# Optimization experiments

Measured on AMD Instinct MI355X. Metric: run time of the kernel, lower is better.

The kernel has to match this reference:

```python
import jax, jax.numpy as jnp
import numpy as np

B, N, DIM, H = 32, 3136, 768, 12
C = DIM // H  # head_dim = 64


def setup_inputs() -> dict:
    key = jax.random.key(0)
    k1, k2, k3, k4 = jax.random.split(key, 4)
    x = jax.random.normal(k1, (B, N, DIM), dtype=jnp.float32)
    # Linear weights stored as (in, out); qkv has no bias (qkv_bias=False)
    w_qkv = jax.random.normal(k2, (DIM, 3 * DIM), dtype=jnp.float32) * (1.0 / np.sqrt(DIM))
    w_proj = jax.random.normal(k3, (DIM, DIM), dtype=jnp.float32) * (1.0 / np.sqrt(DIM))
    b_proj = jax.random.normal(k4, (DIM,), dtype=jnp.float32) * 0.01
    return {"x": x, "w_qkv": w_qkv, "w_proj": w_proj, "b_proj": b_proj}


def reference(x, w_qkv, w_proj, b_proj):
    # qkv projection: [B,N,3*DIM] -> [3,B,H,N,C]
    qkv = (x @ w_qkv).reshape(B, N, 3, H, C).transpose(2, 0, 3, 1, 4)
    q, k, v = qkv[0], qkv[1], qkv[2]
    # Efficient (linear) attention: softmax q over channel dim, k over token dim
    q = jax.nn.softmax(q, axis=-1)                      # [B,H,N,C], softmax over C
    kt = jax.nn.softmax(k.transpose(0, 1, 3, 2), axis=-1)  # [B,H,C,N], softmax over N
    context = jnp.einsum('bhcn,bhnd->bhcd', kt, v)      # [B,H,C,C]
    out = jnp.einsum('bhnc,bhcd->bhnd', q, context)     # [B,H,N,C]
    out = out.transpose(0, 2, 1, 3).reshape(B, N, DIM)  # [B,N,DIM]
    return out @ w_proj + b_proj
```

## Files before the change

kernel.cpp:

```cpp
#include <hip/hip_runtime.h>
#include <hip/hip_bf16.h>

typedef __attribute__((ext_vector_type(8))) short bf16x8;
typedef __attribute__((ext_vector_type(4))) float f32x4;

constexpr int BATCH = 32, SEQ = 3136, DIM = 768, NH = 12, HD = 64;
constexpr int M_TOT = BATCH * SEQ;
constexpr int QKVC  = 3 * DIM;
constexpr int GK    = 768;

__device__ __forceinline__ float bf2f(unsigned short u) {
  union { unsigned int i; float f; } x; x.i = ((unsigned int)u) << 16; return x.f;
}
__device__ __forceinline__ unsigned short f2bf(float f) {
  union { float f; unsigned int i; } x; x.f = f;
  unsigned int r = x.i + 0x7FFFu + ((x.i >> 16) & 1u);
  return (unsigned short)(r >> 16);
}
__device__ __forceinline__ unsigned int pack2(float lo, float hi) {
  return (unsigned int)f2bf(lo) | ((unsigned int)f2bf(hi) << 16);
}
__device__ __forceinline__ void gload_lds16(const unsigned short* g, unsigned short* l) {
  __builtin_amdgcn_global_load_lds(
      (const __attribute__((address_space(1))) void*)g,
      (__attribute__((address_space(3))) void*)l, 16, 0, 0);
}

#define BARX()  asm volatile("s_barrier" ::: "memory")
#define LGKM0() asm volatile("s_waitcnt lgkmcnt(0)" ::: "memory")
#define VM4()   asm volatile("s_waitcnt vmcnt(4)" ::: "memory")
#define SB0()   __builtin_amdgcn_sched_barrier(0)

__global__ void conv_kernel(const float* __restrict__ in, unsigned short* __restrict__ out, long n) {
  long i = ((long)blockIdx.x * blockDim.x + threadIdx.x) * 8;
  long stride = (long)gridDim.x * blockDim.x * 8;
  for (; i < n; i += stride) {
    float4 a = *(const float4*)(in + i);
    float4 b = *(const float4*)(in + i + 4);
    uint4 o;
    o.x = pack2(a.x, a.y); o.y = pack2(a.z, a.w);
    o.z = pack2(b.x, b.y); o.w = pack2(b.z, b.w);
    *(uint4*)(out + i) = o;
  }
}

__global__ void transp_kernel(const float* __restrict__ w, unsigned short* __restrict__ wt, int K, int N) {
  __shared__ float tile[32][33];
  int n0 = blockIdx.x * 32, k0 = blockIdx.y * 32;
  int tx = threadIdx.x, ty = threadIdx.y;
  #pragma unroll
  for (int i = 0; i < 32; i += 8)
    tile[ty + i][tx] = w[(size_t)(k0 + ty + i) * N + n0 + tx];
  __syncthreads();
  #pragma unroll
  for (int i = 0; i < 32; i += 8)
    wt[(size_t)(n0 + ty + i) * K + k0 + tx] = f2bf(tile[tx][ty + i]);
}

__device__ __forceinline__ void stage_half(const unsigned short* __restrict__ G, long row0, int col0,
                                           unsigned short* ldsHalf, int t) {
  int r = t >> 2;
  int gslot = (t & 3) ^ ((t >> 3) & 3);
  char* dst = (char*)ldsHalf + ((t >> 6) << 10);
  gload_lds16(G + (row0 + r) * (long)GK + col0 + gslot * 8, (unsigned short*)dst);
  gload_lds16(G + (row0 + 128 + r) * (long)GK + col0 + gslot * 8, (unsigned short*)(dst + 8192));
}
__device__ __forceinline__ bf16x8 frag(const unsigned short* half, int r, int ko) {
  return *(const bf16x8*)((const char*)half + r * 64 + ((((ko >> 3) ^ ((r >> 1) & 3))) << 4));
}

#define MM16G(Q,A0,A1,A2,A3,B0,B1,B2,B3) do { \
  acc[(Q)+0][0]=__builtin_amdgcn_mfma_f32_16x16x32_bf16(B0,A0,acc[(Q)+0][0],0,0,0); \
  acc[(Q)+0][1]=__builtin_amdgcn_mfma_f32_16x16x32_bf16(B1,A0,acc[(Q)+0][1],0,0,0); \
  acc[(Q)+0][2]=__builtin_amdgcn_mfma_f32_16x16x32_bf16(B2,A0,acc[(Q)+0][2],0,0,0); \
  acc[(Q)+0][3]=__builtin_amdgcn_mfma_f32_16x16x32_bf16(B3,A0,acc[(Q)+0][3],0,0,0); \
  acc[(Q)+1][0]=__builtin_amdgcn_mfma_f32_16x16x32_bf16(B0,A1,acc[(Q)+1][0],0,0,0); \
  acc[(Q)+1][1]=__builtin_amdgcn_mfma_f32_16x16x32_bf16(B1,A1,acc[(Q)+1][1],0,0,0); \
  acc[(Q)+1][2]=__builtin_amdgcn_mfma_f32_16x16x32_bf16(B2,A1,acc[(Q)+1][2],0,0,0); \
  acc[(Q)+1][3]=__builtin_amdgcn_mfma_f32_16x16x32_bf16(B3,A1,acc[(Q)+1][3],0,0,0); \
  acc[(Q)+2][0]=__builtin_amdgcn_mfma_f32_16x16x32_bf16(B0,A2,acc[(Q)+2][0],0,0,0); \
  acc[(Q)+2][1]=__builtin_amdgcn_mfma_f32_16x16x32_bf16(B1,A2,acc[(Q)+2][1],0,0,0); \
  acc[(Q)+2][2]=__builtin_amdgcn_mfma_f32_16x16x32_bf16(B2,A2,acc[(Q)+2][2],0,0,0); \
  acc[(Q)+2][3]=__builtin_amdgcn_mfma_f32_16x16x32_bf16(B3,A2,acc[(Q)+2][3],0,0,0); \
  acc[(Q)+3][0]=__builtin_amdgcn_mfma_f32_16x16x32_bf16(B0,A3,acc[(Q)+3][0],0,0,0); \
  acc[(Q)+3][1]=__builtin_amdgcn_mfma_f32_16x16x32_bf16(B1,A3,acc[(Q)+3][1],0,0,0); \
  acc[(Q)+3][2]=__builtin_amdgcn_mfma_f32_16x16x32_bf16(B2,A3,acc[(Q)+3][2],0,0,0); \
  acc[(Q)+3][3]=__builtin_amdgcn_mfma_f32_16x16x32_bf16(B3,A3,acc[(Q)+3][3],0,0,0); \
} while (0)

#define KTILE_X(BUF, MA2, NB2, C2, MA3, NB3, C3) { \
  const unsigned short* Ah0 = &lds[BUF][0][0][0]; \
  const unsigned short* Ah1 = &lds[BUF][0][1][0]; \
  const unsigned short* Bh1 = &lds[BUF][1][1][0]; \
  const unsigned short* Ah0n = &lds[(BUF) ^ 1][0][0][0]; \
  const unsigned short* Bh0n = &lds[(BUF) ^ 1][1][0][0]; \
   \
  LGKM0(); SB0(); \
  __builtin_amdgcn_s_setprio(1); MM16G(0, a0, a1, a2, a3, b0, b1, b2, b3); \
  __builtin_amdgcn_s_setprio(0); SB0(); \
  a4 = frag(Ah0, ra + 64, ko); a5 = frag(Ah0, ra + 80, ko); \
  a6 = frag(Ah0, ra + 96, ko); a7 = frag(Ah0, ra + 112, ko); \
  b4 = frag(Bh1, rb, ko); b5 = frag(Bh1, rb + 16, ko); \
  stage_half(A, MA2, C2, &lds[(BUF) ^ 1][0][1][0], t); \
  BARX(); \
   \
  LGKM0(); SB0(); \
  __builtin_amdgcn_s_setprio(1); MM16G(4, a4, a5, a6, a7, b0, b1, b2, b3); \
  __builtin_amdgcn_s_setprio(0); SB0(); \
  a0 = frag(Ah1, ra,      ko); a1 = frag(Ah1, ra + 16, ko); \
  a2 = frag(Ah1, ra + 32, ko); a3 = frag(Ah1, ra + 48, ko); \
  b6 = frag(Bh1, rb + 32, ko); b7 = frag(Bh1, rb + 48, ko); \
  stage_half(Bt, NB2, C2, &lds[(BUF) ^ 1][1][1][0], t); \
  VM4(); BARX(); \
   \
  LGKM0(); SB0(); \
  __builtin_amdgcn_s_setprio(1); MM16G(0, a0, a1, a2, a3, b4, b5, b6, b7); \
  __builtin_amdgcn_s_setprio(0); SB0(); \
  a4 = frag(Ah1, ra + 64, ko); a5 = frag(Ah1, ra + 80, ko); \
  a6 = frag(Ah1, ra + 96, ko); a7 = frag(Ah1, ra + 112, ko); \
  b0 = frag(Bh0n, rb, ko); b1 = frag(Bh0n, rb + 16, ko); \
  stage_half(A, MA3, C3, &lds[BUF][0][0][0], t); \
  BARX(); \
   \
  LGKM0(); SB0(); \
  __builtin_amdgcn_s_setprio(1); MM16G(4, a4, a5, a6, a7, b4, b5, b6, b7); \
  __builtin_amdgcn_s_setprio(0); SB0(); \
  a0 = frag(Ah0n, ra,      ko); a1 = frag(Ah0n, ra + 16, ko); \
  a2 = frag(Ah0n, ra + 32, ko); a3 = frag(Ah0n, ra + 48, ko); \
  b2 = frag(Bh0n, rb + 32, ko); b3 = frag(Bh0n, rb + 48, ko); \
  stage_half(Bt, NB3, C3, &lds[BUF][1][0][0], t); \
  VM4(); BARX(); \
}

template<int OUTMODE, int NT>
__global__ __launch_bounds__(512, 2) void gemm256p(const unsigned short* __restrict__ A,
                                                   const unsigned short* __restrict__ Bt,
                                                   void* __restrict__ Cp,
                                                   const float* __restrict__ bias,
                                                   int Nld, int TPX) {
  __shared__ unsigned short lds[2][2][2][8192];
  int t = threadIdx.x, lane = t & 63, wid = t >> 6;
  int wm = wid >> 2, wn = wid & 3;
  int bid = (int)blockIdx.x;
  int xcd = bid & 7, slot = bid >> 3;
  int tau = xcd * TPX + slot;
  int tend = (xcd + 1) * TPX;
  int fl = lane & 15, ko = (lane >> 4) * 8;
  int ra = wm * 128 + fl, rb = wn * 64 + fl;
  f32x4 acc[8][4];
  bf16x8 a0, a1, a2, a3, a4, a5, a6, a7, b0, b1, b2, b3, b4, b5, b6, b7;
  {
    long m0 = (long)(tau / NT) * 256, n0 = (long)(tau % NT) * 256;
    stage_half(A,  m0, 0,  &lds[0][0][0][0], t);
    stage_half(Bt, n0, 0,  &lds[0][1][0][0], t);
    stage_half(A,  m0, 32, &lds[0][0][1][0], t);
    stage_half(Bt, n0, 32, &lds[0][1][1][0], t);
    stage_half(A,  m0, 64, &lds[1][0][0][0], t);
    stage_half(Bt, n0, 64, &lds[1][1][0][0], t);
    VM4(); BARX();
    a0 = frag(&lds[0][0][0][0], ra,      ko); a1 = frag(&lds[0][0][0][0], ra + 16, ko);
    a2 = frag(&lds[0][0][0][0], ra + 32, ko); a3 = frag(&lds[0][0][0][0], ra + 48, ko);
    b0 = frag(&lds[0][1][0][0], rb,      ko); b1 = frag(&lds[0][1][0][0], rb + 16, ko);
    b2 = frag(&lds[0][1][0][0], rb + 32, ko); b3 = frag(&lds[0][1][0][0], rb + 48, ko);
  }
  #pragma unroll 1
  for (; tau < tend; tau += 32) {
    long m0 = (long)(tau / NT) * 256, n0 = (long)(tau % NT) * 256;
    int tn = (tau + 32 < tend) ? tau + 32 : tau;
    long m0n = (long)(tn / NT) * 256, n0n = (long)(tn % NT) * 256;
    #pragma unroll
    for (int i = 0; i < 8; ++i)
      #pragma unroll
      for (int j2 = 0; j2 < 4; ++j2) acc[i][j2] = (f32x4){0.f, 0.f, 0.f, 0.f};
    #pragma unroll 1
    for (int j = 0; j < 10; j += 2) {
      KTILE_X(0, m0, n0, j * 64 + 96,  m0, n0, j * 64 + 128);
      KTILE_X(1, m0, n0, j * 64 + 160, m0, n0, j * 64 + 192);
    }
    KTILE_X(0, m0,  n0,  736, m0n, n0n, 0);
    KTILE_X(1, m0n, n0n, 32,  m0n, n0n, 64);
    int q4 = (lane >> 4) * 4;
    #pragma unroll
    for (int mf = 0; mf < 8; ++mf) {
      long row = m0 + wm * 128 + mf * 16 + fl;
      #pragma unroll
      for (int nf = 0; nf < 4; ++nf) {
        int col = (int)n0 + wn * 64 + nf * 16 + q4;
        if (OUTMODE == 0) {
          unsigned short* C = (unsigned short*)Cp;
          bool doexp = (n0 < 2 * DIM);
          float v0 = acc[mf][nf][0], v1 = acc[mf][nf][1], v2 = acc[mf][nf][2], v3 = acc[mf][nf][3];
          if (doexp) { v0 = __expf(v0); v1 = __expf(v1); v2 = __expf(v2); v3 = __expf(v3); }
          uint2 o; o.x = pack2(v0, v1); o.y = pack2(v2, v3);
          *(uint2*)(C + (size_t)row * Nld + col) = o;
        } else {
          float* C = (float*)Cp;
          float4 bb = *(const float4*)(bias + col);
          float4 o = { acc[mf][nf][0] + bb.x, acc[mf][nf][1] + bb.y,
                       acc[mf][nf][2] + bb.z, acc[mf][nf][3] + bb.w };
          *(float4*)(C + (size_t)row * Nld + col) = o;
        }
      }
    }
  }
}

__global__ void ctx_part(const unsigned short* __restrict__ qkv, float* __restrict__ part,
                         float* __restrict__ dpart) {
  int blk = blockIdx.x;
  int bh = blk / 7, ch = blk - bh * 7;
  int b = bh / NH, h = bh % NH;
  __shared__ unsigned short Et[64 * 40];
  __shared__ unsigned short Vt[64 * 40];
  __shared__ float denom[64];
  int t = threadIdx.x, lane = t & 63, w = t >> 6;
  if (t < 64) denom[t] = 0.0f;
  int nl = t >> 3, e0 = (t & 7) * 8;
  int ko = (lane >> 4) * 8, fl = lane & 15;
  size_t base = (size_t)b * SEQ * QKVC + (size_t)h * HD;
  float dp[8] = {};
  f32x4 acc[4] = {};
  int c0b = ch * 448;
  for (int c0 = c0b; c0 < c0b + 448; c0 += 32) {
    __syncthreads();
    size_t rb = base + (size_t)(c0 + nl) * QKVC;
    uint4 kvec = *(const uint4*)(qkv + rb + DIM + e0);
    uint4 vvec = *(const uint4*)(qkv + rb + 2 * DIM + e0);
    const unsigned short* kp = (const unsigned short*)&kvec;
    const unsigned short* vp = (const unsigned short*)&vvec;
    #pragma unroll
    for (int j = 0; j < 8; ++j) {
      dp[j] += bf2f(kp[j]);
      Et[(e0 + j) * 40 + nl] = kp[j];
      Vt[(e0 + j) * 40 + nl] = vp[j];
    }
    __syncthreads();
    bf16x8 af = *(const bf16x8*)(Et + (w * 16 + fl) * 40 + ko);
    #pragma unroll
    for (int nf = 0; nf < 4; ++nf) {
      bf16x8 bv = *(const bf16x8*)(Vt + (nf * 16 + fl) * 40 + ko);
      acc[nf] = __builtin_amdgcn_mfma_f32_16x16x32_bf16(af, bv, acc[nf], 0, 0, 0);
    }
  }
  #pragma unroll
  for (int j = 0; j < 8; ++j) atomicAdd(&denom[e0 + j], dp[j]);
  __syncthreads();
  int r0 = (lane >> 4) * 4;
  float* pp = part + (size_t)blk * 4096;
  #pragma unroll
  for (int nf = 0; nf < 4; ++nf)
    #pragma unroll
    for (int r = 0; r < 4; ++r) {
      int c = w * 16 + r0 + r;
      int d = nf * 16 + fl;
      pp[d * 64 + c] = acc[nf][r];
    }
  if (t < 64) dpart[blk * 64 + t] = denom[t];
}

__global__ void ctx_reduce(const float* __restrict__ part, const float* __restrict__ dpart,
                           unsigned short* __restrict__ ctxT) {
  int bh = blockIdx.x, t = threadIdx.x;
  const float* pp = part + (size_t)bh * 7 * 4096;
  const float* dd = dpart + (size_t)bh * 7 * 64;
  #pragma unroll
  for (int i = 0; i < 16; ++i) {
    int idx = i * 256 + t;
    float s = 0.f, ds = 0.f;
    #pragma unroll
    for (int c = 0; c < 7; ++c) {
      s += pp[c * 4096 + idx];
      ds += dd[c * 64 + (idx & 63)];
    }
    ctxT[(size_t)bh * 4096 + idx] = f2bf(s / ds);
  }
}

__global__ void pv_kernel(const unsigned short* __restrict__ qkv, const unsigned short* __restrict__ ctxT,
                          unsigned short* __restrict__ aout) {
  int bid = blockIdx.x;
  int bh = bid / 49, chunk = bid - bh * 49;
  int b = bh / NH, h = bh % NH;
  int n0 = chunk * 64;
  __shared__ unsigned short P[64 * 80];
  __shared__ unsigned short CT[64 * 80];
  __shared__ float srow[64];
  int t = threadIdx.x, lane = t & 63, w = t >> 6;
  int ko = (lane >> 4) * 8, fl = lane & 15;
  if (t < 64) srow[t] = 0.0f;
  {
    int d = t >> 2, cq = (t & 3) * 16;
    const uint4* src = (const uint4*)(ctxT + (size_t)bh * 4096 + d * 64 + cq);
    *(uint4*)(CT + d * 80 + cq) = src[0];
    *(uint4*)(CT + d * 80 + cq + 8) = src[1];
  }
  __syncthreads();
  {
    int nl = t >> 2, cq = (t & 3) * 16;
    size_t rb = (size_t)(b * SEQ + n0 + nl) * QKVC + h * HD + cq;
    uint4 q0 = *(const uint4*)(qkv + rb);
    uint4 q1 = *(const uint4*)(qkv + rb + 8);
    *(uint4*)(P + nl * 80 + cq) = q0;
    *(uint4*)(P + nl * 80 + cq + 8) = q1;
    const unsigned short* qp0 = (const unsigned short*)&q0;
    const unsigned short* qp1 = (const unsigned short*)&q1;
    float s = 0.0f;
    #pragma unroll
    for (int j = 0; j < 8; ++j) s += bf2f(qp0[j]) + bf2f(qp1[j]);
    atomicAdd(&srow[nl], s);
  }
  __syncthreads();
  f32x4 acc[4] = {};
  #pragma unroll
  for (int kk = 0; kk < 2; ++kk) {
    bf16x8 af = *(const bf16x8*)(P + (w * 16 + fl) * 80 + kk * 32 + ko);
    #pragma unroll
    for (int nf = 0; nf < 4; ++nf) {
      bf16x8 bv = *(const bf16x8*)(CT + (nf * 16 + fl) * 80 + kk * 32 + ko);
      acc[nf] = __builtin_amdgcn_mfma_f32_16x16x32_bf16(af, bv, acc[nf], 0, 0, 0);
    }
  }
  int r0 = (lane >> 4) * 4;
  #pragma unroll
  for (int nf = 0; nf < 4; ++nf)
    #pragma unroll
    for (int r = 0; r < 4; ++r) {
      int nlr = w * 16 + r0 + r;
      int d = nf * 16 + fl;
      float v = acc[nf][r] / srow[nlr];
      aout[(size_t)(b * SEQ + n0 + nlr) * DIM + h * HD + d] = f2bf(v);
    }
}

extern "C" void kernel_launch(void* const* d_in, const int* in_sizes, int n_in,
                              void* d_out, int out_size, void* d_ws, size_t ws_size,
                              hipStream_t stream) {
  const float* x      = (const float*)d_in[0];
  const float* w_qkv  = (const float*)d_in[1];
  const float* w_proj = (const float*)d_in[2];
  const float* b_proj = (const float*)d_in[3];
  char* ws = (char*)d_ws;
  unsigned short* x_bf    = (unsigned short*)(ws);
  unsigned short* wt_qkv  = (unsigned short*)(ws + 154140672);
  unsigned short* wt_proj = (unsigned short*)(ws + 157679616);
  unsigned short* qkv     = (unsigned short*)(ws + 158859264);
  unsigned short* ctxT    = (unsigned short*)(ws + 154140672);
  float* part  = (float*)(ws);
  float* dpart = (float*)(ws + 44040192);
  unsigned short* aout = (unsigned short*)(ws);

  conv_kernel<<<2048, 256, 0, stream>>>(x, x_bf, (long)M_TOT * DIM);
  transp_kernel<<<dim3(QKVC / 32, DIM / 32), dim3(32, 8), 0, stream>>>(w_qkv, wt_qkv, DIM, QKVC);
  transp_kernel<<<dim3(DIM / 32, DIM / 32), dim3(32, 8), 0, stream>>>(w_proj, wt_proj, DIM, DIM);
  gemm256p<0, 9><<<256, 512, 0, stream>>>(x_bf, wt_qkv, qkv, nullptr, QKVC, 441);
  ctx_part<<<BATCH * NH * 7, 256, 0, stream>>>(qkv, part, dpart);
  ctx_reduce<<<BATCH * NH, 256, 0, stream>>>(part, dpart, ctxT);
  pv_kernel<<<BATCH * NH * (SEQ / 64), 256, 0, stream>>>(qkv, ctxT, aout);
  gemm256p<1, 3><<<256, 512, 0, stream>>>(aout, wt_proj, (float*)d_out, b_proj, DIM, 147);
}
```

Baseline: 860.6 us.

## Interleave LDS fragment reads with MFMAs in GEMM and merge prep kernels

The GEMM k-tile body is restructured so global-to-LDS staging is issued at the start of each quarter step, and LDS fragment loads are interleaved between groups of four MFMAs. The vmcnt waits are loosened (vmcnt 6/8) to keep more loads in flight. The goal is to hide LDS read latency behind matrix work and deepen memory pipelining. Separately, the bf16 conversion and the two weight-transpose kernels are merged into one launch to cut launch overhead. The new wait counts and barrier placement change the synchronisation assumptions, which could introduce races if the in-flight counts are wrong.

```diff
diff --git a/kernel.cpp b/kernel.cpp
--- a/kernel.cpp
+++ b/kernel.cpp
@@ -28,33 +28,44 @@
 
 #define BARX()  asm volatile("s_barrier" ::: "memory")
 #define LGKM0() asm volatile("s_waitcnt lgkmcnt(0)" ::: "memory")
-#define VM4()   asm volatile("s_waitcnt vmcnt(4)" ::: "memory")
+#define VM8()   asm volatile("s_waitcnt vmcnt(8)" ::: "memory")
+#define VM6()   asm volatile("s_waitcnt vmcnt(6)" ::: "memory")
 #define SB0()   __builtin_amdgcn_sched_barrier(0)
 
-__global__ void conv_kernel(const float* __restrict__ in, unsigned short* __restrict__ out, long n) {
-  long i = ((long)blockIdx.x * blockDim.x + threadIdx.x) * 8;
-  long stride = (long)gridDim.x * blockDim.x * 8;
-  for (; i < n; i += stride) {
-    float4 a = *(const float4*)(in + i);
-    float4 b = *(const float4*)(in + i + 4);
-    uint4 o;
-    o.x = pack2(a.x, a.y); o.y = pack2(a.z, a.w);
-    o.z = pack2(b.x, b.y); o.w = pack2(b.z, b.w);
-    *(uint4*)(out + i) = o;
-  }
-}
-
-__global__ void transp_kernel(const float* __restrict__ w, unsigned short* __restrict__ wt, int K, int N) {
+__global__ void prep_kernel(const float* __restrict__ x, unsigned short* __restrict__ x_bf,
+                            const float* __restrict__ w_qkv, unsigned short* __restrict__ wt_qkv,
+                            const float* __restrict__ w_proj, unsigned short* __restrict__ wt_proj) {
   __shared__ float tile[32][33];
-  int n0 = blockIdx.x * 32, k0 = blockIdx.y * 32;
-  int tx = threadIdx.x, ty = threadIdx.y;
-  #pragma unroll
-  for (int i = 0; i < 32; i += 8)
-    tile[ty + i][tx] = w[(size_t)(k0 + ty + i) * N + n0 + tx];
-  __syncthreads();
-  #pragma unroll
-  for (int i = 0; i < 32; i += 8)
-    wt[(size_t)(n0 + ty + i) * K + k0 + tx] = f2bf(tile[tx][ty + i]);
+  int bid = blockIdx.x, t = threadIdx.x;
+  if (bid < 2048) {
+    long n = (long)M_TOT * DIM;
+    long i = ((long)bid * 256 + t) * 8;
+    long stride = (long)2048 * 256 * 8;
+    for (; i < n; i += stride) {
+      float4 a = *(const float4*)(x + i);
+      float4 b = *(const float4*)(x + i + 4);
+      uint4 o;
+      o.x = pack2(a.x, a.y); o.y = pack2(a.z, a.w);
+      o.z = pack2(b.x, b.y); o.w = pack2(b.z, b.w);
+      *(uint4*)(x_bf + i) = o;
+    }
+  } else {
+    const float* w; unsigned short* wt; int N, bx, by;
+    if (bid < 2048 + 1728) {
+      int r = bid - 2048; w = w_qkv; wt = wt_qkv; N = QKVC; bx = r % 72; by = r / 72;
+    } else {
+      int r = bid - 3776; w = w_proj; wt = wt_proj; N = DIM; bx = r % 24; by = r / 24;
+    }
+    int n0 = bx * 32, k0 = by * 32;
+    int tx = t & 31, ty = t >> 5;
+    #pragma unroll
+    for (int i = 0; i < 32; i += 8)
+      tile[ty + i][tx] = w[(size_t)(k0 + ty + i) * N + n0 + tx];
+    __syncthreads();
+    #pragma unroll
+    for (int i = 0; i < 32; i += 8)
+      wt[(size_t)(n0 + ty + i) * GK + k0 + tx] = f2bf(tile[tx][ty + i]);
+  }
 }
 
 __device__ __forceinline__ void stage_half(const unsigned short* __restrict__ G, long row0, int col0,
@@ -69,67 +80,71 @@
   return *(const bf16x8*)((const char*)half + r * 64 + ((((ko >> 3) ^ ((r >> 1) & 3))) << 4));
 }
 
-#define MM16G(Q,A0,A1,A2,A3,B0,B1,B2,B3) do { \
-  acc[(Q)+0][0]=__builtin_amdgcn_mfma_f32_16x16x32_bf16(B0,A0,acc[(Q)+0][0],0,0,0); \
-  acc[(Q)+0][1]=__builtin_amdgcn_mfma_f32_16x16x32_bf16(B1,A0,acc[(Q)+0][1],0,0,0); \
-  acc[(Q)+0][2]=__builtin_amdgcn_mfma_f32_16x16x32_bf16(B2,A0,acc[(Q)+0][2],0,0,0); \
-  acc[(Q)+0][3]=__builtin_amdgcn_mfma_f32_16x16x32_bf16(B3,A0,acc[(Q)+0][3],0,0,0); \
-  acc[(Q)+1][0]=__builtin_amdgcn_mfma_f32_16x16x32_bf16(B0,A1,acc[(Q)+1][0],0,0,0); \
-  acc[(Q)+1][1]=__builtin_amdgcn_mfma_f32_16x16x32_bf16(B1,A1,acc[(Q)+1][1],0,0,0); \
-  acc[(Q)+1][2]=__builtin_amdgcn_mfma_f32_16x16x32_bf16(B2,A1,acc[(Q)+1][2],0,0,0); \
-  acc[(Q)+1][3]=__builtin_amdgcn_mfma_f32_16x16x32_bf16(B3,A1,acc[(Q)+1][3],0,0,0); \
-  acc[(Q)+2][0]=__builtin_amdgcn_mfma_f32_16x16x32_bf16(B0,A2,acc[(Q)+2][0],0,0,0); \
-  acc[(Q)+2][1]=__builtin_amdgcn_mfma_f32_16x16x32_bf16(B1,A2,acc[(Q)+2][1],0,0,0); \
-  acc[(Q)+2][2]=__builtin_amdgcn_mfma_f32_16x16x32_bf16(B2,A2,acc[(Q)+2][2],0,0,0); \
-  acc[(Q)+2][3]=__builtin_amdgcn_mfma_f32_16x16x32_bf16(B3,A2,acc[(Q)+2][3],0,0,0); \
-  acc[(Q)+3][0]=__builtin_amdgcn_mfma_f32_16x16x32_bf16(B0,A3,acc[(Q)+3][0],0,0,0); \
-  acc[(Q)+3][1]=__builtin_amdgcn_mfma_f32_16x16x32_bf16(B1,A3,acc[(Q)+3][1],0,0,0); \
-  acc[(Q)+3][2]=__builtin_amdgcn_mfma_f32_16x16x32_bf16(B2,A3,acc[(Q)+3][2],0,0,0); \
-  acc[(Q)+3][3]=__builtin_amdgcn_mfma_f32_16x16x32_bf16(B3,A3,acc[(Q)+3][3],0,0,0); \
+#define MM4S(QM,AV,B0,B1,B2,B3) do { \
+  acc[QM][0]=__builtin_amdgcn_mfma_f32_16x16x32_bf16(B0,AV,acc[QM][0],0,0,0); \
+  acc[QM][1]=__builtin_amdgcn_mfma_f32_16x16x32_bf16(B1,AV,acc[QM][1],0,0,0); \
+  acc[QM][2]=__builtin_amdgcn_mfma_f32_16x16x32_bf16(B2,AV,acc[QM][2],0,0,0); \
+  acc[QM][3]=__builtin_amdgcn_mfma_f32_16x16x32_bf16(B3,AV,acc[QM][3],0,0,0); \
 } while (0)
 
-#define KTILE_X(BUF, MA2, NB2, C2, MA3, NB3, C3) { \
+#define KTILE_I(BUF, MA2, NB2, C2, MA3, NB3, C3) { \
   const unsigned short* Ah0 = &lds[BUF][0][0][0]; \
   const unsigned short* Ah1 = &lds[BUF][0][1][0]; \
   const unsigned short* Bh1 = &lds[BUF][1][1][0]; \
   const unsigned short* Ah0n = &lds[(BUF) ^ 1][0][0][0]; \
   const unsigned short* Bh0n = &lds[(BUF) ^ 1][1][0][0]; \
    \
+  stage_half(A, MA2, C2, &lds[(BUF) ^ 1][0][1][0], t); \
   LGKM0(); SB0(); \
-  __builtin_amdgcn_s_setprio(1); MM16G(0, a0, a1, a2, a3, b0, b1, b2, b3); \
+  __builtin_amdgcn_s_setprio(1); \
+  MM4S(0, a0, b0, b1, b2, b3); SB0(); \
+  a4 = frag(Ah0, ra + 64, ko); a5 = frag(Ah0, ra + 80, ko); SB0(); \
+  MM4S(1, a1, b0, b1, b2, b3); SB0(); \
+  a6 = frag(Ah0, ra + 96, ko); a7 = frag(Ah0, ra + 112, ko); SB0(); \
+  MM4S(2, a2, b0, b1, b2, b3); \
+  MM4S(3, a3, b0, b1, b2, b3); \
   __builtin_amdgcn_s_setprio(0); SB0(); \
-  a4 = frag(Ah0, ra + 64, ko); a5 = frag(Ah0, ra + 80, ko); \
-  a6 = frag(Ah0, ra + 96, ko); a7 = frag(Ah0, ra + 112, ko); \
-  b4 = frag(Bh1, rb, ko); b5 = frag(Bh1, rb + 16, ko); \
-  stage_half(A, MA2, C2, &lds[(BUF) ^ 1][0][1][0], t); \
+  VM6(); BARX(); \
+   \
+  stage_half(Bt, NB2, C2, &lds[(BUF) ^ 1][1][1][0], t); \
+  LGKM0(); SB0(); \
+  __builtin_amdgcn_s_setprio(1); \
+  MM4S(4, a4, b0, b1, b2, b3); SB0(); \
+  a0 = frag(Ah1, ra,      ko); a1 = frag(Ah1, ra + 16, ko); \
+  a2 = frag(Ah1, ra + 32, ko); a3 = frag(Ah1, ra + 48, ko); SB0(); \
+  MM4S(5, a5, b0, b1, b2, b3); SB0(); \
+  b4 = frag(Bh1, rb, ko); b5 = frag(Bh1, rb + 16, ko); SB0(); \
+  MM4S(6, a6, b0, b1, b2, b3); SB0(); \
+  b6 = frag(Bh1, rb + 32, ko); b7 = frag(Bh1, rb + 48, ko); SB0(); \
+  MM4S(7, a7, b0, b1, b2, b3); \
+  __builtin_amdgcn_s_setprio(0); SB0(); \
   BARX(); \
    \
+  stage_half(A, MA3, C3, &lds[BUF][0][0][0], t); \
   LGKM0(); SB0(); \
-  __builtin_amdgcn_s_setprio(1); MM16G(4, a4, a5, a6, a7, b0, b1, b2, b3); \
+  __builtin_amdgcn_s_setprio(1); \
+  MM4S(0, a0, b4, b5, b6, b7); SB0(); \
+  a4 = frag(Ah1, ra + 64, ko); a5 = frag(Ah1, ra + 80, ko); SB0(); \
+  MM4S(1, a1, b4, b5, b6, b7); SB0(); \
+  a6 = frag(Ah1, ra + 96, ko); a7 = frag(Ah1, ra + 112, ko); SB0(); \
+  MM4S(2, a2, b4, b5, b6, b7); \
+  MM4S(3, a3, b4, b5, b6, b7); \
   __builtin_amdgcn_s_setprio(0); SB0(); \
-  a0 = frag(Ah1, ra,      ko); a1 = frag(Ah1, ra + 16, ko); \
-  a2 = frag(Ah1, ra + 32, ko); a3 = frag(Ah1, ra + 48, ko); \
-  b6 = frag(Bh1, rb + 32, ko); b7 = frag(Bh1, rb + 48, ko); \
-  stage_half(Bt, NB2, C2, &lds[(BUF) ^ 1][1][1][0], t); \
-  VM4(); BARX(); \
+  VM6(); BARX(); \
    \
+  stage_half(Bt, NB3, C3, &lds[BUF][1][0][0], t); \
   LGKM0(); SB0(); \
-  __builtin_amdgcn_s_setprio(1); MM16G(0, a0, a1, a2, a3, b4, b5, b6, b7); \
+  __builtin_amdgcn_s_setprio(1); \
+  MM4S(4, a4, b4, b5, b6, b7); SB0(); \
+  a0 = frag(Ah0n, ra,      ko); a1 = frag(Ah0n, ra + 16, ko); \
+  a2 = frag(Ah0n, ra + 32, ko); a3 = frag(Ah0n, ra + 48, ko); SB0(); \
+  MM4S(5, a5, b4, b5, b6, b7); SB0(); \
+  b0 = frag(Bh0n, rb, ko); b1 = frag(Bh0n, rb + 16, ko); SB0(); \
+  MM4S(6, a6, b4, b5, b6, b7); SB0(); \
+  b2 = frag(Bh0n, rb + 32, ko); b3 = frag(Bh0n, rb + 48, ko); SB0(); \
+  MM4S(7, a7, b4, b5, b6, b7); \
   __builtin_amdgcn_s_setprio(0); SB0(); \
-  a4 = frag(Ah1, ra + 64, ko); a5 = frag(Ah1, ra + 80, ko); \
-  a6 = frag(Ah1, ra + 96, ko); a7 = frag(Ah1, ra + 112, ko); \
-  b0 = frag(Bh0n, rb, ko); b1 = frag(Bh0n, rb + 16, ko); \
-  stage_half(A, MA3, C3, &lds[BUF][0][0][0], t); \
   BARX(); \
-   \
-  LGKM0(); SB0(); \
-  __builtin_amdgcn_s_setprio(1); MM16G(4, a4, a5, a6, a7, b4, b5, b6, b7); \
-  __builtin_amdgcn_s_setprio(0); SB0(); \
-  a0 = frag(Ah0n, ra,      ko); a1 = frag(Ah0n, ra + 16, ko); \
-  a2 = frag(Ah0n, ra + 32, ko); a3 = frag(Ah0n, ra + 48, ko); \
-  b2 = frag(Bh0n, rb + 32, ko); b3 = frag(Bh0n, rb + 48, ko); \
-  stage_half(Bt, NB3, C3, &lds[BUF][1][0][0], t); \
-  VM4(); BARX(); \
 }
 
 template<int OUTMODE, int NT>
@@ -157,7 +172,7 @@
     stage_half(Bt, n0, 32, &lds[0][1][1][0], t);
     stage_half(A,  m0, 64, &lds[1][0][0][0], t);
     stage_half(Bt, n0, 64, &lds[1][1][0][0], t);
-    VM4(); BARX();
+    VM8(); BARX();
     a0 = frag(&lds[0][0][0][0], ra,      ko); a1 = frag(&lds[0][0][0][0], ra + 16, ko);
     a2 = frag(&lds[0][0][0][0], ra + 32, ko); a3 = frag(&lds[0][0][0][0], ra + 48, ko);
     b0 = frag(&lds[0][1][0][0], rb,      ko); b1 = frag(&lds[0][1][0][0], rb + 16, ko);
@@ -174,11 +189,11 @@
       for (int j2 = 0; j2 < 4; ++j2) acc[i][j2] = (f32x4){0.f, 0.f, 0.f, 0.f};
     #pragma unroll 1
     for (int j = 0; j < 10; j += 2) {
-      KTILE_X(0, m0, n0, j * 64 + 96,  m0, n0, j * 64 + 128);
-      KTILE_X(1, m0, n0, j * 64 + 160, m0, n0, j * 64 + 192);
-    }
-    KTILE_X(0, m0,  n0,  736, m0n, n0n, 0);
-    KTILE_X(1, m0n, n0n, 32,  m0n, n0n, 64);
+      KTILE_I(0, m0, n0, j * 64 + 96,  m0, n0, j * 64 + 128);
+      KTILE_I(1, m0, n0, j * 64 + 160, m0, n0, j * 64 + 192);
+    }
+    KTILE_I(0, m0,  n0,  736, m0n, n0n, 0);
+    KTILE_I(1, m0n, n0n, 32,  m0n, n0n, 64);
     int q4 = (lane >> 4) * 4;
     #pragma unroll
     for (int mf = 0; mf < 8; ++mf) {
@@ -349,9 +364,7 @@
   float* dpart = (float*)(ws + 44040192);
   unsigned short* aout = (unsigned short*)(ws);
 
-  conv_kernel<<<2048, 256, 0, stream>>>(x, x_bf, (long)M_TOT * DIM);
-  transp_kernel<<<dim3(QKVC / 32, DIM / 32), dim3(32, 8), 0, stream>>>(w_qkv, wt_qkv, DIM, QKVC);
-  transp_kernel<<<dim3(DIM / 32, DIM / 32), dim3(32, 8), 0, stream>>>(w_proj, wt_proj, DIM, DIM);
+  prep_kernel<<<4352, 256, 0, stream>>>(x, x_bf, w_qkv, wt_qkv, w_proj, wt_proj);
   gemm256p<0, 9><<<256, 512, 0, stream>>>(x_bf, wt_qkv, qkv, nullptr, QKVC, 441);
   ctx_part<<<BATCH * NH * 7, 256, 0, stream>>>(qkv, part, dpart);
   ctx_reduce<<<BATCH * NH, 256, 0, stream>>>(part, dpart, ctxT);
```

Measured after the change: 918.2 us. 6.7% more time.

## Merge prep kernels into one launch and relax GEMM vmcnt waits

Applied to the files above, without the earlier changes.

Combines the fp32-to-bf16 conversion of x and the two weight transposes into a single prep kernel launch, removing two launch gaps. In the 256x256 GEMM main loop, the B-fragment LDS reads are moved later so that each vmcnt wait sits at the A-half stages and allows more outstanding global loads (vmcnt 6/8 instead of 4). The goal is deeper load-compute overlap with fewer stalls. The risk is a correctness race if the wait counts no longer cover the LDS halves being read.

```diff
diff --git a/kernel.cpp b/kernel.cpp
--- a/kernel.cpp
+++ b/kernel.cpp
@@ -28,33 +28,44 @@
 
 #define BARX()  asm volatile("s_barrier" ::: "memory")
 #define LGKM0() asm volatile("s_waitcnt lgkmcnt(0)" ::: "memory")
-#define VM4()   asm volatile("s_waitcnt vmcnt(4)" ::: "memory")
+#define VM8()   asm volatile("s_waitcnt vmcnt(8)" ::: "memory")
+#define VM6()   asm volatile("s_waitcnt vmcnt(6)" ::: "memory")
 #define SB0()   __builtin_amdgcn_sched_barrier(0)
 
-__global__ void conv_kernel(const float* __restrict__ in, unsigned short* __restrict__ out, long n) {
-  long i = ((long)blockIdx.x * blockDim.x + threadIdx.x) * 8;
-  long stride = (long)gridDim.x * blockDim.x * 8;
-  for (; i < n; i += stride) {
-    float4 a = *(const float4*)(in + i);
-    float4 b = *(const float4*)(in + i + 4);
-    uint4 o;
-    o.x = pack2(a.x, a.y); o.y = pack2(a.z, a.w);
-    o.z = pack2(b.x, b.y); o.w = pack2(b.z, b.w);
-    *(uint4*)(out + i) = o;
-  }
-}
-
-__global__ void transp_kernel(const float* __restrict__ w, unsigned short* __restrict__ wt, int K, int N) {
+__global__ void prep_kernel(const float* __restrict__ x, unsigned short* __restrict__ x_bf,
+                            const float* __restrict__ w_qkv, unsigned short* __restrict__ wt_qkv,
+                            const float* __restrict__ w_proj, unsigned short* __restrict__ wt_proj) {
   __shared__ float tile[32][33];
-  int n0 = blockIdx.x * 32, k0 = blockIdx.y * 32;
-  int tx = threadIdx.x, ty = threadIdx.y;
-  #pragma unroll
-  for (int i = 0; i < 32; i += 8)
-    tile[ty + i][tx] = w[(size_t)(k0 + ty + i) * N + n0 + tx];
-  __syncthreads();
-  #pragma unroll
-  for (int i = 0; i < 32; i += 8)
-    wt[(size_t)(n0 + ty + i) * K + k0 + tx] = f2bf(tile[tx][ty + i]);
+  int bid = blockIdx.x, t = threadIdx.x;
+  if (bid < 2048) {
+    long n = (long)M_TOT * DIM;
+    long i = ((long)bid * 256 + t) * 8;
+    long stride = (long)2048 * 256 * 8;
+    for (; i < n; i += stride) {
+      float4 a = *(const float4*)(x + i);
+      float4 b = *(const float4*)(x + i + 4);
+      uint4 o;
+      o.x = pack2(a.x, a.y); o.y = pack2(a.z, a.w);
+      o.z = pack2(b.x, b.y); o.w = pack2(b.z, b.w);
+      *(uint4*)(x_bf + i) = o;
+    }
+  } else {
+    const float* w; unsigned short* wt; int N, bx, by;
+    if (bid < 2048 + 1728) {
+      int r = bid - 2048; w = w_qkv; wt = wt_qkv; N = QKVC; bx = r % 72; by = r / 72;
+    } else {
+      int r = bid - 3776; w = w_proj; wt = wt_proj; N = DIM; bx = r % 24; by = r / 24;
+    }
+    int n0 = bx * 32, k0 = by * 32;
+    int tx = t & 31, ty = t >> 5;
+    #pragma unroll
+    for (int i = 0; i < 32; i += 8)
+      tile[ty + i][tx] = w[(size_t)(k0 + ty + i) * N + n0 + tx];
+    __syncthreads();
+    #pragma unroll
+    for (int i = 0; i < 32; i += 8)
+      wt[(size_t)(n0 + ty + i) * GK + k0 + tx] = f2bf(tile[tx][ty + i]);
+  }
 }
 
 __device__ __forceinline__ void stage_half(const unsigned short* __restrict__ G, long row0, int col0,
@@ -88,10 +99,10 @@
   acc[(Q)+3][3]=__builtin_amdgcn_mfma_f32_16x16x32_bf16(B3,A3,acc[(Q)+3][3],0,0,0); \
 } while (0)
 
-#define KTILE_X(BUF, MA2, NB2, C2, MA3, NB3, C3) { \
+#define KTILE_W(BUF, MA2, NB2, C2, MA3, NB3, C3) { \
   const unsigned short* Ah0 = &lds[BUF][0][0][0]; \
+  const unsigned short* Bh1 = &lds[BUF][1][1][0]; \
   const unsigned short* Ah1 = &lds[BUF][0][1][0]; \
-  const unsigned short* Bh1 = &lds[BUF][1][1][0]; \
   const unsigned short* Ah0n = &lds[(BUF) ^ 1][0][0][0]; \
   const unsigned short* Bh0n = &lds[(BUF) ^ 1][1][0][0]; \
    \
@@ -100,36 +111,36 @@
   __builtin_amdgcn_s_setprio(0); SB0(); \
   a4 = frag(Ah0, ra + 64, ko); a5 = frag(Ah0, ra + 80, ko); \
   a6 = frag(Ah0, ra + 96, ko); a7 = frag(Ah0, ra + 112, ko); \
-  b4 = frag(Bh1, rb, ko); b5 = frag(Bh1, rb + 16, ko); \
   stage_half(A, MA2, C2, &lds[(BUF) ^ 1][0][1][0], t); \
-  BARX(); \
+  VM6(); BARX(); \
    \
   LGKM0(); SB0(); \
   __builtin_amdgcn_s_setprio(1); MM16G(4, a4, a5, a6, a7, b0, b1, b2, b3); \
   __builtin_amdgcn_s_setprio(0); SB0(); \
   a0 = frag(Ah1, ra,      ko); a1 = frag(Ah1, ra + 16, ko); \
   a2 = frag(Ah1, ra + 32, ko); a3 = frag(Ah1, ra + 48, ko); \
+  b4 = frag(Bh1, rb,      ko); b5 = frag(Bh1, rb + 16, ko); \
   b6 = frag(Bh1, rb + 32, ko); b7 = frag(Bh1, rb + 48, ko); \
   stage_half(Bt, NB2, C2, &lds[(BUF) ^ 1][1][1][0], t); \
-  VM4(); BARX(); \
+  BARX(); \
    \
   LGKM0(); SB0(); \
   __builtin_amdgcn_s_setprio(1); MM16G(0, a0, a1, a2, a3, b4, b5, b6, b7); \
   __builtin_amdgcn_s_setprio(0); SB0(); \
   a4 = frag(Ah1, ra + 64, ko); a5 = frag(Ah1, ra + 80, ko); \
   a6 = frag(Ah1, ra + 96, ko); a7 = frag(Ah1, ra + 112, ko); \
-  b0 = frag(Bh0n, rb, ko); b1 = frag(Bh0n, rb + 16, ko); \
   stage_half(A, MA3, C3, &lds[BUF][0][0][0], t); \
-  BARX(); \
+  VM6(); BARX(); \
    \
   LGKM0(); SB0(); \
   __builtin_amdgcn_s_setprio(1); MM16G(4, a4, a5, a6, a7, b4, b5, b6, b7); \
   __builtin_amdgcn_s_setprio(0); SB0(); \
   a0 = frag(Ah0n, ra,      ko); a1 = frag(Ah0n, ra + 16, ko); \
   a2 = frag(Ah0n, ra + 32, ko); a3 = frag(Ah0n, ra + 48, ko); \
+  b0 = frag(Bh0n, rb,      ko); b1 = frag(Bh0n, rb + 16, ko); \
   b2 = frag(Bh0n, rb + 32, ko); b3 = frag(Bh0n, rb + 48, ko); \
   stage_half(Bt, NB3, C3, &lds[BUF][1][0][0], t); \
-  VM4(); BARX(); \
+  BARX(); \
 }
 
 template<int OUTMODE, int NT>
@@ -157,7 +168,7 @@
     stage_half(Bt, n0, 32, &lds[0][1][1][0], t);
     stage_half(A,  m0, 64, &lds[1][0][0][0], t);
     stage_half(Bt, n0, 64, &lds[1][1][0][0], t);
-    VM4(); BARX();
+    VM8(); BARX();
     a0 = frag(&lds[0][0][0][0], ra,      ko); a1 = frag(&lds[0][0][0][0], ra + 16, ko);
     a2 = frag(&lds[0][0][0][0], ra + 32, ko); a3 = frag(&lds[0][0][0][0], ra + 48, ko);
     b0 = frag(&lds[0][1][0][0], rb,      ko); b1 = frag(&lds[0][1][0][0], rb + 16, ko);
@@ -174,11 +185,11 @@
       for (int j2 = 0; j2 < 4; ++j2) acc[i][j2] = (f32x4){0.f, 0.f, 0.f, 0.f};
     #pragma unroll 1
     for (int j = 0; j < 10; j += 2) {
-      KTILE_X(0, m0, n0, j * 64 + 96,  m0, n0, j * 64 + 128);
-      KTILE_X(1, m0, n0, j * 64 + 160, m0, n0, j * 64 + 192);
-    }
-    KTILE_X(0, m0,  n0,  736, m0n, n0n, 0);
-    KTILE_X(1, m0n, n0n, 32,  m0n, n0n, 64);
+      KTILE_W(0, m0, n0, j * 64 + 96,  m0, n0, j * 64 + 128);
+      KTILE_W(1, m0, n0, j * 64 + 160, m0, n0, j * 64 + 192);
+    }
+    KTILE_W(0, m0,  n0,  736, m0n, n0n, 0);
+    KTILE_W(1, m0n, n0n, 32,  m0n, n0n, 64);
     int q4 = (lane >> 4) * 4;
     #pragma unroll
     for (int mf = 0; mf < 8; ++mf) {
@@ -349,9 +360,7 @@
   float* dpart = (float*)(ws + 44040192);
   unsigned short* aout = (unsigned short*)(ws);
 
-  conv_kernel<<<2048, 256, 0, stream>>>(x, x_bf, (long)M_TOT * DIM);
-  transp_kernel<<<dim3(QKVC / 32, DIM / 32), dim3(32, 8), 0, stream>>>(w_qkv, wt_qkv, DIM, QKVC);
-  transp_kernel<<<dim3(DIM / 32, DIM / 32), dim3(32, 8), 0, stream>>>(w_proj, wt_proj, DIM, DIM);
+  prep_kernel<<<4352, 256, 0, stream>>>(x, x_bf, w_qkv, wt_qkv, w_proj, wt_proj);
   gemm256p<0, 9><<<256, 512, 0, stream>>>(x_bf, wt_qkv, qkv, nullptr, QKVC, 441);
   ctx_part<<<BATCH * NH * 7, 256, 0, stream>>>(qkv, part, dpart);
   ctx_reduce<<<BATCH * NH, 256, 0, stream>>>(part, dpart, ctxT);
```

Result: no change. 858.2 us (-0.3%).
